# Performance work log

Hardware: AMD Instinct MI355X
Metric: run time of the kernel (lower is better)

The kernel has to match this reference:

```python
import jax, jax.numpy as jnp
import numpy as np

B, G, C = 32, 50, 80
IMG = 640
STRIDES = (8, 16, 32)
CENTER_RADIUS = 2.5


def _make_grids():
    xs, ys, ss = [], [], []
    for s in STRIDES:
        n = IMG // s
        yv, xv = np.meshgrid(np.arange(n, dtype=np.float32), np.arange(n, dtype=np.float32), indexing='ij')
        xs.append(xv.reshape(-1)); ys.append(yv.reshape(-1))
        ss.append(np.full(n * n, s, dtype=np.float32))
    return np.concatenate(xs), np.concatenate(ys), np.concatenate(ss)


def setup_inputs():
    xg, yg, sg = _make_grids()
    A = xg.shape[0]  # 8400
    ks = jax.random.split(jax.random.key(0), 5)
    # decoded box predictions near grid centers (cxcywh, pixel units)
    ctr = jnp.stack([jnp.asarray((xg + 0.5) * sg), jnp.asarray((yg + 0.5) * sg)], -1)[None] \
        + jax.random.normal(ks[0], (B, A, 2)) * 8.0
    wh = jnp.exp(jax.random.normal(ks[1], (B, A, 2)) * 0.5) * jnp.asarray(sg)[None, :, None] * 4.0
    pred_output = jnp.concatenate([ctr, wh, jax.random.normal(ks[2], (B, A, 1 + C))], -1)  # [B,A,85]
    obj_preds = jax.random.normal(ks[3], (B, A, 1))
    cls_preds = jax.random.normal(ks[4], (B, A, C))
    # labels [B,G,5] = (class, cx, cy, w, h); first num_gt rows valid, rest zero
    rng = np.random.RandomState(0)
    lab = np.zeros((B, G, 5), np.float32)
    for b in range(B):
        ng = rng.randint(5, G)
        lab[b, :ng, 0] = rng.randint(0, C, ng)
        lab[b, :ng, 1:3] = rng.uniform(40.0, IMG - 40.0, (ng, 2))
        lab[b, :ng, 3:5] = rng.uniform(20.0, 160.0, (ng, 2))
    return {"pred_output": pred_output, "obj_preds": obj_preds, "cls_preds": cls_preds,
            "labels": jnp.asarray(lab), "x_shifts": jnp.asarray(xg),
            "y_shifts": jnp.asarray(yg), "strides": jnp.asarray(sg)}


def _pairwise_iou_cxcywh(a, b):
    # a [G,4], b [A,4] -> [G,A]
    tl = jnp.maximum(a[:, None, :2] - a[:, None, 2:] * 0.5, b[None, :, :2] - b[None, :, 2:] * 0.5)
    br = jnp.minimum(a[:, None, :2] + a[:, None, 2:] * 0.5, b[None, :, :2] + b[None, :, 2:] * 0.5)
    area_a = a[:, 2] * a[:, 3]
    area_b = b[:, 2] * b[:, 3]
    en = jnp.all(tl < br, -1).astype(a.dtype)
    area_i = jnp.prod(br - tl, -1) * en
    return area_i / (area_a[:, None] + area_b[None, :] - area_i + 1e-16)


def _assign_one(gt, gt_valid, boxes, cls_logit, obj_logit, xg, yg, sg):
    # SimOTA assignment for a single image, fully vectorized over [G,A].
    # gt [G,5], gt_valid [G], boxes [A,4], cls_logit [A,C], obj_logit [A,1]
    num_gt = gt.shape[0]
    gt_cls = gt[:, 0].astype(jnp.int32)
    gb = gt[:, 1:5]
    xc = (xg + 0.5) * sg
    yc = (yg + 0.5) * sg
    d_box = jnp.stack([
        xc[None, :] - (gb[:, 0:1] - gb[:, 2:3] * 0.5),
        (gb[:, 0:1] + gb[:, 2:3] * 0.5) - xc[None, :],
        yc[None, :] - (gb[:, 1:2] - gb[:, 3:4] * 0.5),
        (gb[:, 1:2] + gb[:, 3:4] * 0.5) - yc[None, :]], -1)
    in_boxes = (jnp.min(d_box, -1) > 0) & gt_valid[:, None]
    d_ctr = jnp.stack([
        xc[None, :] - (gb[:, 0:1] - CENTER_RADIUS * sg[None, :]),
        (gb[:, 0:1] + CENTER_RADIUS * sg[None, :]) - xc[None, :],
        yc[None, :] - (gb[:, 1:2] - CENTER_RADIUS * sg[None, :]),
        (gb[:, 1:2] + CENTER_RADIUS * sg[None, :]) - yc[None, :]], -1)
    in_ctr = (jnp.min(d_ctr, -1) > 0) & gt_valid[:, None]
    fg0 = jnp.any(in_boxes | in_ctr, 0)           # [A] candidate anchors (fg_mask)
    and_ctr = in_boxes & in_ctr                    # [G,A]
    ious = _pairwise_iou_cxcywh(gb, boxes) * fg0[None, :].astype(boxes.dtype) * gt_valid[:, None].astype(boxes.dtype)
    # pairwise BCE(sqrt(sig(cls)*sig(obj)), one_hot) summed over classes, without [G,A,C]
    logq = 0.5 * (jax.nn.log_sigmoid(cls_logit) + jax.nn.log_sigmoid(obj_logit))  # [A,C]
    q = jnp.clip(jnp.exp(logq), 1e-7, 1.0 - 1e-7)
    s_neg = jnp.sum(jnp.log1p(-q), -1)             # [A] sum_c log(1-q_c)
    q_gt = q[:, gt_cls].T                          # [G,A]
    cls_cost = -jnp.log(q_gt) + jnp.log1p(-q_gt) - s_neg[None, :]
    invalid = (~fg0)[None, :] | (~gt_valid)[:, None]
    cost = cls_cost - 3.0 * jnp.log(ious + 1e-8) + 1e5 * (~and_ctr) + 1e9 * invalid
    # dynamic-k: sum of top-10 ious per gt, truncated, min 1
    dyn_k = jnp.maximum(jnp.sum(jax.lax.top_k(ious, 10)[0], -1).astype(jnp.int32), 1)  # [G]
    ranks = jnp.argsort(jnp.argsort(cost, 1), 1)   # rank of each anchor in ascending cost
    matching = (ranks < dyn_k[:, None]) & gt_valid[:, None]
    # resolve anchors claimed by >1 gt: keep min-cost gt
    best_gt = jnp.argmin(cost, 0)                  # [A]
    onehot_best = jnp.arange(num_gt)[:, None] == best_gt[None, :]
    matching = jnp.where(jnp.sum(matching, 0)[None, :] > 1, onehot_best, matching)
    fg = jnp.any(matching, 0)                      # [A] final fg mask
    matched = jnp.argmax(matching, 0)              # [A] matched gt index
    pred_iou = jnp.sum(matching * ious, 0)         # [A]
    cls_t = jax.nn.one_hot(gt_cls[matched], cls_logit.shape[-1], dtype=boxes.dtype) \
        * (pred_iou * fg.astype(boxes.dtype))[:, None]
    return cls_t, fg, matched


def _forward(pred_output, obj_preds, cls_preds, labels, x_shifts, y_shifts, strides):
    bbox = pred_output[:, :, :4]
    gt_valid = labels.sum(-1) > 0
    cls_t, fg, matched = jax.vmap(_assign_one, in_axes=(0, 0, 0, 0, 0, None, None, None))(
        labels, gt_valid, bbox, cls_preds, obj_preds, x_shifts, y_shifts, strides)
    cls_t = jax.lax.stop_gradient(cls_t)  # get_assignments is @torch.no_grad()
    reg_t = jnp.take_along_axis(labels[:, :, 1:5], matched[:, :, None], axis=1)  # [B,A,4]
    fg_f = fg.astype(pred_output.dtype)
    num_fg = jnp.maximum(jnp.sum(fg_f), 1.0)
    # IoU loss (cxcywh), loss = 1 - iou^2, only on fg anchors
    tl = jnp.maximum(bbox[..., :2] - bbox[..., 2:] * 0.5, reg_t[..., :2] - reg_t[..., 2:] * 0.5)
    br = jnp.minimum(bbox[..., :2] + bbox[..., 2:] * 0.5, reg_t[..., :2] + reg_t[..., 2:] * 0.5)
    en = jnp.all(tl < br, -1).astype(bbox.dtype)
    area_i = jnp.prod(br - tl, -1) * en
    area_u = bbox[..., 2] * bbox[..., 3] + reg_t[..., 2] * reg_t[..., 3] - area_i
    iou = area_i / (area_u + 1e-16)
    loss_iou = jnp.sum((1.0 - iou ** 2) * fg_f) / num_fg
    bce = lambda x, y: jax.nn.softplus(x) - x * y  # BCEWithLogits, reduction='none'
    loss_obj = jnp.sum(bce(obj_preds[..., 0], fg_f)) / num_fg
    loss_cls = jnp.sum(bce(cls_preds, cls_t) * fg_f[..., None]) / num_fg
    return 5.0 * loss_iou + loss_obj + loss_cls


def reference(pred_output, obj_preds, cls_preds, labels, x_shifts, y_shifts, strides):
    return _forward(pred_output, obj_preds, cls_preds, labels, x_shifts, y_shifts, strides)
```

## Files before the change

### kernel.cpp

```cpp
#include <hip/hip_runtime.h>
#include <cstdint>
#include <cstddef>

#define BB 32
#define GG 50
#define CC 80
#define AA 8400
#define PCH (5 + CC)
#define NLB ((BB * AA + 255) / 256)
#define NXCD 8
#define FGBIT 63
#define SENTC 3.3e38f
#define SENTI 0x7fffffff

__device__ __forceinline__ float logsig_fast(float x) {
    float e = __expf(-fabsf(x));
    return fminf(x, 0.f) - __logf(1.f + e);
}
__device__ __forceinline__ void sp_ls(float x, float& sp, float& ls) {
    float e = __expf(-fabsf(x));
    float l = __logf(1.f + e);
    sp = fmaxf(x, 0.f) + l;
    ls = fminf(x, 0.f) - l;
}
__device__ __forceinline__ float softplusf(float x) {
    return fmaxf(x, 0.f) + log1pf(expf(-fabsf(x)));
}

__device__ __forceinline__ float pair_iou(float px, float py, float pw, float ph,
                                          float gx, float gy, float gw, float gh) {
    float tlx = fmaxf(gx - gw * 0.5f, px - pw * 0.5f);
    float tly = fmaxf(gy - gh * 0.5f, py - ph * 0.5f);
    float brx = fminf(gx + gw * 0.5f, px + pw * 0.5f);
    float bry = fminf(gy + gh * 0.5f, py + ph * 0.5f);
    float en = (tlx < brx && tly < bry) ? 1.f : 0.f;
    float ai = (brx - tlx) * (bry - tly) * en;
    return ai / (gw * gh + pw * ph - ai + 1e-16f);
}
__device__ __forceinline__ float cost_val(float x , float lo ,
                                          float sn , float v ,
                                          bool ac, bool f0, bool valid) {
    float lq = 0.5f * (logsig_fast(x) + lo);
    float q = fminf(fmaxf(__expf(lq), 1e-7f), 1.f - 1e-7f);
    float cst = -__logf(q) + __logf(1.f - q) - sn;
    cst -= 3.0f * __logf(v + 1e-8f);
    cst += 100000.0f * (ac ? 0.f : 1.f);
    cst += 1000000000.0f * ((!f0 || !valid) ? 1.f : 0.f);
    return cst;
}

__global__ __launch_bounds__(256)
void k_precompute(const float* __restrict__ pred, const float* __restrict__ obj,
                  const float* __restrict__ cls,
                  float2* __restrict__ lsn, float* __restrict__ sps,
                  float4* __restrict__ pbox) {
    int t = blockIdx.x * blockDim.x + threadIdx.x;
    int i = t >> 2;
    int sub = t & 3;
    if (i >= BB * AA) return;
    float lo = logsig_fast(obj[i]);
    const float4* c4 = (const float4*)(cls + (size_t)i * CC);
    float sn = 0.f, sp = 0.f;
#pragma unroll
    for (int j = 0; j < 5; j++) {
        float4 v = c4[sub + 4 * j];
        float xs4[4] = {v.x, v.y, v.z, v.w};
#pragma unroll
        for (int u = 0; u < 4; u++) {
            float x = xs4[u];
            float spx, lsx;
            sp_ls(x, spx, lsx);
            sp += spx;
            float q = __expf(0.5f * (lsx + lo));
            q = fminf(fmaxf(q, 1e-7f), 1.f - 1e-7f);
            sn += __logf(1.f - q);
        }
    }
    sp += __shfl_xor(sp, 1); sn += __shfl_xor(sn, 1);
    sp += __shfl_xor(sp, 2); sn += __shfl_xor(sn, 2);
    float pv = pred[(size_t)i * PCH + sub];
    ((float*)pbox)[(size_t)i * 4 + sub] = pv;
    if (sub == 0) {
        lsn[i] = make_float2(lo, sn);
        sps[i] = sp;
    }
}

__global__ void k_geom(const float* __restrict__ labels, const float* __restrict__ xs,
                       const float* __restrict__ ys, const float* __restrict__ ss,
                       unsigned long long* __restrict__ amask) {
    int b = blockIdx.y;
    int a = blockIdx.x * blockDim.x + threadIdx.x;
    __shared__ float lab[GG * 5];
    __shared__ int lv[GG];
    for (int t = threadIdx.x; t < GG * 5; t += blockDim.x) lab[t] = labels[b * GG * 5 + t];
    __syncthreads();
    if (threadIdx.x < GG) {
        const float* r = lab + threadIdx.x * 5;
        lv[threadIdx.x] = ((r[0] + r[1] + r[2] + r[3] + r[4]) > 0.f) ? 1 : 0;
    }
    __syncthreads();
    if (a >= AA) return;
    float s = ss[a];
    float xc = (xs[a] + 0.5f) * s;
    float yc = (ys[a] + 0.5f) * s;
    unsigned long long m = 0;
    int any = 0;
    for (int g = 0; g < GG; g++) {
        if (!lv[g]) continue;
        const float* r = lab + g * 5;
        float gx = r[1], gy = r[2], gw = r[3], gh = r[4];
        float d1 = xc - (gx - gw * 0.5f);
        float d2 = (gx + gw * 0.5f) - xc;
        float d3 = yc - (gy - gh * 0.5f);
        float d4 = (gy + gh * 0.5f) - yc;
        bool ib = fminf(fminf(d1, d2), fminf(d3, d4)) > 0.f;
        float cr = 2.5f * s;
        float e1 = xc - (gx - cr);
        float e2 = (gx + cr) - xc;
        float e3 = yc - (gy - cr);
        float e4 = (gy + cr) - yc;
        bool ic = fminf(fminf(e1, e2), fminf(e3, e4)) > 0.f;
        if (ib || ic) any = 1;
        if (ib && ic) m |= 1ull << g;
    }
    if (any) m |= 1ull << FGBIT;
    amask[b * AA + a] = m;
}

__global__ __launch_bounds__(256)
void k_assign(const float4* __restrict__ pbox, const float2* __restrict__ lsn,
              const float* __restrict__ cls,
              const unsigned long long* __restrict__ amask,
              const float* __restrict__ labels,
              unsigned long long* __restrict__ mmask) {
    int bid = blockIdx.x;
    int w = (bid % NXCD) * (BB * GG / NXCD) + bid / NXCD;
    int b = w / GG, g = w % GG;
    const float* r = labels + (size_t)w * 5;
    float gcls = r[0], gx = r[1], gy = r[2], gw = r[3], gh = r[4];
    if (!((gcls + gx + gy + gw + gh) > 0.f)) return;
    int gtc = (int)gcls;
    int tid = threadIdx.x;
    int lane = tid & 63;
    int wv = tid >> 6;

    float ivl[10];
    float cvl[10];
    int   cil[10];
#pragma unroll
    for (int t = 0; t < 10; t++) { ivl[t] = 0.f; cvl[t] = SENTC; cil[t] = SENTI; }
    int nac = 0;

    const int chunk = AA / 4;
    int abase = wv * chunk, aend = abase + chunk;

    for (int a0 = abase; a0 < aend; a0 += 64) {
        int a = a0 + lane;
        bool inr = a < aend;
        int ia = b * AA + (inr ? a : (aend - 1));
        unsigned long long am = amask[ia];
        bool f0 = inr && ((am >> FGBIT) & 1ull);
        bool ac = inr && ((am >> g) & 1ull);
        nac += __popcll(__ballot(ac));
        float v = 0.f;
        if (f0) {
            float4 pb = pbox[ia];
            v = pair_iou(pb.x, pb.y, pb.z, pb.w, gx, gy, gw, gh);
        }
        {
            float mv = v;
            while (true) {
                unsigned long long mb = __ballot(mv > ivl[9]);
                if (!mb) break;
                int src = __ffsll(mb) - 1;
                float bv = __shfl(mv, src);
#pragma unroll
                for (int t = 0; t < 10; t++)
                    if (bv > ivl[t]) { float tmp = ivl[t]; ivl[t] = bv; bv = tmp; }
                if (lane == src) mv = -1.f;
            }
        }
        {
            float c = SENTC; int id = SENTI;
            if (ac) {
                float x = cls[(size_t)ia * CC + gtc];
                float2 ls = lsn[ia];
                c = cost_val(x, ls.x, ls.y, v, true, true, true);
                id = a;
            }
            while (true) {
                bool enter = (c < cvl[9]) || (c == cvl[9] && id < cil[9]);
                unsigned long long mb = __ballot(enter);
                if (!mb) break;
                int src = __ffsll(mb) - 1;
                float bc = __shfl(c, src);
                int bi = __shfl(id, src);
#pragma unroll
                for (int t = 0; t < 10; t++) {
                    bool sw = (bc < cvl[t]) || (bc == cvl[t] && bi < cil[t]);
                    if (sw) {
                        float tf = cvl[t]; cvl[t] = bc; bc = tf;
                        int ti = cil[t]; cil[t] = bi; bi = ti;
                    }
                }
                if (lane == src) { c = SENTC; id = SENTI; }
            }
        }
    }

    __shared__ float IV[4][10];
    __shared__ float CV[4][10];
    __shared__ int CI[4][10];
    __shared__ int NAC[4];
    __shared__ int s_k, s_n0;
    __shared__ int sel[10];

    if (lane == 0) {
#pragma unroll
        for (int t = 0; t < 10; t++) { IV[wv][t] = ivl[t]; CV[wv][t] = cvl[t]; CI[wv][t] = cil[t]; }
        NAC[wv] = nac;
    }
    __syncthreads();
    if (tid == 0) {
        int h[4] = {0, 0, 0, 0};
        float ssum = 0.f;
        for (int j = 0; j < 10; j++) {
            float bv = -1.f; int bc = 0;
#pragma unroll
            for (int c2 = 0; c2 < 4; c2++)
                if (h[c2] < 10 && IV[c2][h[c2]] > bv) { bv = IV[c2][h[c2]]; bc = c2; }
            ssum += bv;
            h[bc]++;
        }
        int k = (int)ssum;
        if (k < 1) k = 1;
        s_k = k;
        s_n0 = NAC[0] + NAC[1] + NAC[2] + NAC[3];
    }
    __syncthreads();
    int k = s_k;

    if (s_n0 < k) {
#pragma unroll
        for (int t = 0; t < 10; t++) { cvl[t] = SENTC; cil[t] = SENTI; }
        for (int a0 = abase; a0 < aend; a0 += 64) {
            int a = a0 + lane;
            bool inr = a < aend;
            int ia = b * AA + (inr ? a : (aend - 1));
            unsigned long long am = amask[ia];
            bool f0 = inr && ((am >> FGBIT) & 1ull);
            bool ac = inr && ((am >> g) & 1ull);
            float v = 0.f;
            if (f0) {
                float4 pb = pbox[ia];
                v = pair_iou(pb.x, pb.y, pb.z, pb.w, gx, gy, gw, gh);
            }
            float c = SENTC; int id = SENTI;
            if (inr) {
                float x = cls[(size_t)ia * CC + gtc];
                float2 ls = lsn[ia];
                c = cost_val(x, ls.x, ls.y, v, ac, f0, true);
                id = a;
            }
            while (true) {
                bool enter = (c < cvl[9]) || (c == cvl[9] && id < cil[9]);
                unsigned long long mb = __ballot(enter);
                if (!mb) break;
                int src = __ffsll(mb) - 1;
                float bc = __shfl(c, src);
                int bi = __shfl(id, src);
#pragma unroll
                for (int t = 0; t < 10; t++) {
                    bool sw = (bc < cvl[t]) || (bc == cvl[t] && bi < cil[t]);
                    if (sw) {
                        float tf = cvl[t]; cvl[t] = bc; bc = tf;
                        int ti = cil[t]; cil[t] = bi; bi = ti;
                    }
                }
                if (lane == src) { c = SENTC; id = SENTI; }
            }
        }
        if (lane == 0) {
#pragma unroll
            for (int t = 0; t < 10; t++) { CV[wv][t] = cvl[t]; CI[wv][t] = cil[t]; }
        }
        __syncthreads();
    }

    if (tid == 0) {
        int h[4] = {0, 0, 0, 0};
        for (int j = 0; j < k; j++) {
            float bv = SENTC; int bix = SENTI; int bc = 0;
#pragma unroll
            for (int c2 = 0; c2 < 4; c2++) {
                if (h[c2] < 10) {
                    float av = CV[c2][h[c2]]; int ax = CI[c2][h[c2]];
                    if (av < bv || (av == bv && ax < bix)) { bv = av; bix = ax; bc = c2; }
                }
            }
            sel[j] = bix;
            h[bc]++;
        }
    }
    __syncthreads();
    if (tid < k) {
        atomicOr(&mmask[(size_t)b * AA + sel[tid]], 1ull << g);
    }
}

__global__ void k_loss(const float4* __restrict__ pbox, const float* __restrict__ obj,
                       const float* __restrict__ cls, const float* __restrict__ labels,
                       const float2* __restrict__ lsn,
                       const unsigned long long* __restrict__ amask,
                       const unsigned long long* __restrict__ mmask,
                       const float* __restrict__ sps, float* __restrict__ partial) {
    int i = blockIdx.x * blockDim.x + threadIdx.x;
    float li = 0.f, lo = 0.f, lc = 0.f, nf = 0.f;
    if (i < BB * AA) {
        int b = i / AA, a = i % AA;
        unsigned long long m = mmask[i];
        int cnt = __popcll(m);
        bool fg = (m != 0);
        int mg = 0;
        float4 pb = pbox[i];
        unsigned long long am = amask[i];
        bool f0 = (am >> FGBIT) & 1ull;
        if (cnt > 1) {
            float2 ls = lsn[i];
            float bv = 3.4e38f;
            for (int g = 0; g < GG; g++) {
                const float* r = labels + (size_t)(b * GG + g) * 5;
                float gcls = r[0], gx = r[1], gy = r[2], gw = r[3], gh = r[4];
                bool valid = (gcls + gx + gy + gw + gh) > 0.f;
                int gtc = (int)gcls;
                float raw = pair_iou(pb.x, pb.y, pb.z, pb.w, gx, gy, gw, gh);
                float v = raw * (f0 ? 1.f : 0.f) * (valid ? 1.f : 0.f);
                float x = cls[(size_t)i * CC + gtc];
                bool ac = (am >> g) & 1ull;
                float cst = cost_val(x, ls.x, ls.y, v, ac, f0, valid);
                if (cst < bv) { bv = cst; mg = g; }
            }
        } else if (cnt == 1) {
            mg = __ffsll((unsigned long long)m) - 1;
        }
        float o = obj[i];
        lo = softplusf(o) - (fg ? o : 0.f);
        if (fg) {
            const float* r = labels + (size_t)(b * GG + mg) * 5;
            float gcls = r[0], gx = r[1], gy = r[2], gw = r[3], gh = r[4];
            bool valid = (gcls + gx + gy + gw + gh) > 0.f;
            int gtc = (int)gcls;
            float piou = pair_iou(pb.x, pb.y, pb.z, pb.w, gx, gy, gw, gh)
                         * (f0 ? 1.f : 0.f) * (valid ? 1.f : 0.f);
            float tlx = fmaxf(pb.x - pb.z * 0.5f, gx - gw * 0.5f);
            float tly = fmaxf(pb.y - pb.w * 0.5f, gy - gh * 0.5f);
            float brx = fminf(pb.x + pb.z * 0.5f, gx + gw * 0.5f);
            float bry = fminf(pb.y + pb.w * 0.5f, gy + gh * 0.5f);
            float en = (tlx < brx && tly < bry) ? 1.f : 0.f;
            float ai = (brx - tlx) * (bry - tly) * en;
            float u = pb.z * pb.w + gw * gh - ai;
            float v2 = ai / (u + 1e-16f);
            li = 1.f - v2 * v2;
            lc = sps[i] - cls[(size_t)i * CC + gtc] * piou;
            nf = 1.f;
        }
    }
    for (int off = 32; off; off >>= 1) {
        li += __shfl_down(li, off);
        lo += __shfl_down(lo, off);
        lc += __shfl_down(lc, off);
        nf += __shfl_down(nf, off);
    }
    __shared__ float red[4][4];
    int wid = threadIdx.x >> 6;
    if ((threadIdx.x & 63) == 0) {
        red[wid][0] = li; red[wid][1] = lo; red[wid][2] = lc; red[wid][3] = nf;
    }
    __syncthreads();
    if (threadIdx.x == 0) {
        float s0 = 0.f, s1 = 0.f, s2 = 0.f, s3 = 0.f;
#pragma unroll
        for (int t = 0; t < 4; t++) {
            s0 += red[t][0]; s1 += red[t][1]; s2 += red[t][2]; s3 += red[t][3];
        }
        float4* pb = (float4*)partial;
        pb[blockIdx.x] = make_float4(s0, s1, s2, s3);
    }
}

__global__ void k_final(const float* __restrict__ partial, float* __restrict__ out) {
    int tid = threadIdx.x;
    float s0 = 0.f, s1 = 0.f, s2 = 0.f, s3 = 0.f;
    const float4* pb = (const float4*)partial;
    for (int i = tid; i < NLB; i += 256) {
        float4 v = pb[i];
        s0 += v.x; s1 += v.y; s2 += v.z; s3 += v.w;
    }
    for (int off = 32; off; off >>= 1) {
        s0 += __shfl_down(s0, off);
        s1 += __shfl_down(s1, off);
        s2 += __shfl_down(s2, off);
        s3 += __shfl_down(s3, off);
    }
    __shared__ float red[4][4];
    int wid = tid >> 6;
    if ((tid & 63) == 0) {
        red[wid][0] = s0; red[wid][1] = s1; red[wid][2] = s2; red[wid][3] = s3;
    }
    __syncthreads();
    if (tid == 0) {
        float li = 0.f, lo = 0.f, lc = 0.f, nf = 0.f;
#pragma unroll
        for (int t = 0; t < 4; t++) {
            li += red[t][0]; lo += red[t][1]; lc += red[t][2]; nf += red[t][3];
        }
        nf = fmaxf(nf, 1.f);
        out[0] = (5.f * li + lo + lc) / nf;
    }
}

extern "C" void kernel_launch(void* const* d_in, const int* in_sizes, int n_in,
                              void* d_out, int out_size, void* d_ws, size_t ws_size,
                              hipStream_t stream) {
    const float* pred = (const float*)d_in[0];
    const float* obj  = (const float*)d_in[1];
    const float* cls  = (const float*)d_in[2];
    const float* lab  = (const float*)d_in[3];
    const float* xs   = (const float*)d_in[4];
    const float* ys   = (const float*)d_in[5];
    const float* ss   = (const float*)d_in[6];
    float* out = (float*)d_out;

    const size_t BA = (size_t)BB * AA;

    float2* lsn  = (float2*)d_ws;
    float*  sps  = (float*)(lsn + BA);
    float4* pbox = (float4*)(sps + BA);
    unsigned long long* amask = (unsigned long long*)(pbox + BA);
    unsigned long long* mmask = amask + BA;
    float* partial = (float*)(mmask + BA);

    hipMemsetAsync(mmask, 0, BA * sizeof(unsigned long long), stream);

    dim3 blk(256);
    k_precompute<<<dim3((BB * AA * 4 + 255) / 256), blk, 0, stream>>>(pred, obj, cls,
                                                                      lsn, sps, pbox);
    k_geom<<<dim3((AA + 255) / 256, BB), blk, 0, stream>>>(lab, xs, ys, ss, amask);
    k_assign<<<dim3(BB * GG), blk, 0, stream>>>(pbox, lsn, cls, amask, lab, mmask);
    k_loss<<<dim3(NLB), blk, 0, stream>>>(pbox, obj, cls, lab, lsn, amask,
                                          mmask, sps, partial);
    k_final<<<1, blk, 0, stream>>>(partial, out);
}
```

Baseline: 164.3 us.

## Compact candidate anchors per image in k_geom and iterate only them in k_assign

k_geom now appends, per image, the indices of anchors with a nonzero geometry mask to a compacted list, using a wave-level ballot plus one atomic per wave. The first pass of k_assign loops over this list instead of all 8400 anchors, so far fewer anchors go through IoU top-k and cost top-k for each GT. The list order is nondeterministic because of the atomics, which could change tie-breaking in the top-k selection. It also adds a second memset and more workspace, and the fallback pass still scans the full range.

Measured after the change: 177.6 us. 8.1% more time.

```diff
diff --git a/kernel.cpp b/kernel.cpp
--- a/kernel.cpp
+++ b/kernel.cpp
@@ -88,7 +88,8 @@
 
 __global__ void k_geom(const float* __restrict__ labels, const float* __restrict__ xs,
                        const float* __restrict__ ys, const float* __restrict__ ss,
-                       unsigned long long* __restrict__ amask) {
+                       unsigned long long* __restrict__ amask,
+                       int* __restrict__ clist, int* __restrict__ ccnt) {
     int b = blockIdx.y;
     int a = blockIdx.x * blockDim.x + threadIdx.x;
     __shared__ float lab[GG * 5];
@@ -126,6 +127,18 @@
     }
     if (any) m |= 1ull << FGBIT;
     amask[b * AA + a] = m;
+    int lane = threadIdx.x & 63;
+    unsigned long long act = __ballot(m != 0);
+    if (act) {
+        int leader = __ffsll(act) - 1;
+        int base = 0;
+        if (lane == leader) base = atomicAdd(&ccnt[b], __popcll(act));
+        base = __shfl(base, leader);
+        if (m != 0) {
+            int off = __popcll(act & ((1ull << lane) - 1ull));
+            clist[b * AA + base + off] = a;
+        }
+    }
 }
 
 __global__ __launch_bounds__(256)
@@ -133,6 +146,7 @@
               const float* __restrict__ cls,
               const unsigned long long* __restrict__ amask,
               const float* __restrict__ labels,
+              const int* __restrict__ clist, const int* __restrict__ ccnt,
               unsigned long long* __restrict__ mmask) {
     int bid = blockIdx.x;
     int w = (bid % NXCD) * (BB * GG / NXCD) + bid / NXCD;
@@ -144,6 +158,7 @@
     int tid = threadIdx.x;
     int lane = tid & 63;
     int wv = tid >> 6;
+    int cnt = ccnt[b];
 
     float ivl[10];
     float cvl[10];
@@ -152,22 +167,17 @@
     for (int t = 0; t < 10; t++) { ivl[t] = 0.f; cvl[t] = SENTC; cil[t] = SENTI; }
     int nac = 0;
 
-    const int chunk = AA / 4;
-    int abase = wv * chunk, aend = abase + chunk;
-
-    for (int a0 = abase; a0 < aend; a0 += 64) {
-        int a = a0 + lane;
-        bool inr = a < aend;
-        int ia = b * AA + (inr ? a : (aend - 1));
+    for (int i0 = wv * 64; i0 < cnt; i0 += 256) {
+        int i = i0 + lane;
+        bool inr = i < cnt;
+        int a = clist[b * AA + (inr ? i : (cnt - 1))];
+        int ia = b * AA + a;
         unsigned long long am = amask[ia];
+        float4 pb = pbox[ia];
         bool f0 = inr && ((am >> FGBIT) & 1ull);
         bool ac = inr && ((am >> g) & 1ull);
         nac += __popcll(__ballot(ac));
-        float v = 0.f;
-        if (f0) {
-            float4 pb = pbox[ia];
-            v = pair_iou(pb.x, pb.y, pb.z, pb.w, gx, gy, gw, gh);
-        }
+        float v = f0 ? pair_iou(pb.x, pb.y, pb.z, pb.w, gx, gy, gw, gh) : 0.f;
         {
             float mv = v;
             while (true) {
@@ -242,6 +252,8 @@
     int k = s_k;
 
     if (s_n0 < k) {
+        const int chunk = AA / 4;
+        int abase = wv * chunk, aend = abase + chunk;
 #pragma unroll
         for (int t = 0; t < 10; t++) { cvl[t] = SENTC; cil[t] = SENTI; }
         for (int a0 = abase; a0 < aend; a0 += 64) {
@@ -440,14 +452,19 @@
     unsigned long long* amask = (unsigned long long*)(pbox + BA);
     unsigned long long* mmask = amask + BA;
     float* partial = (float*)(mmask + BA);
+    int* clist = (int*)(partial + (size_t)NLB * 4);
+    int* ccnt  = clist + BA;
 
     hipMemsetAsync(mmask, 0, BA * sizeof(unsigned long long), stream);
+    hipMemsetAsync(ccnt, 0, BB * sizeof(int), stream);
 
     dim3 blk(256);
     k_precompute<<<dim3((BB * AA * 4 + 255) / 256), blk, 0, stream>>>(pred, obj, cls,
                                                                       lsn, sps, pbox);
-    k_geom<<<dim3((AA + 255) / 256, BB), blk, 0, stream>>>(lab, xs, ys, ss, amask);
-    k_assign<<<dim3(BB * GG), blk, 0, stream>>>(pbox, lsn, cls, amask, lab, mmask);
+    k_geom<<<dim3((AA + 255) / 256, BB), blk, 0, stream>>>(lab, xs, ys, ss, amask,
+                                                           clist, ccnt);
+    k_assign<<<dim3(BB * GG), blk, 0, stream>>>(pbox, lsn, cls, amask, lab,
+                                                clist, ccnt, mmask);
     k_loss<<<dim3(NLB), blk, 0, stream>>>(pbox, obj, cls, lab, lsn, amask,
                                           mmask, sps, partial);
     k_final<<<1, blk, 0, stream>>>(partial, out);
```
